# Performance work log

Measured on AMD Instinct MI355X. Metric: run time of the kernel, lower is better.

The kernel has to match this reference:

```python
import jax, jax.numpy as jnp
import numpy as np

LORA_ALPHA = 32.0
LORA_R = 16
SCALING = LORA_ALPHA / LORA_R


def setup_inputs() -> dict:
    key = jax.random.key(0)
    k1, k2, k3, k4, k5, k6 = jax.random.split(key, 6)
    B, S, D_IN, D_OUT = 4, 2048, 4096, 4096
    x = jax.random.normal(k1, (B, S, D_IN), dtype=jnp.float32)
    # int8 weight stored as int8 (spec uses int32 range [-127,127])
    qweight = jax.random.randint(k2, (D_OUT, D_IN), -127, 128, dtype=jnp.int32).astype(jnp.int8)
    # per-output-channel dequant scales (bf16 in torch; fp32 here for reference fidelity)
    scales = jax.random.uniform(k3, (D_OUT,), dtype=jnp.float32, minval=0.5, maxval=1.5) * 0.01
    bias = jax.random.normal(k4, (D_OUT,), dtype=jnp.float32) * 0.02
    # kaiming-uniform-like init for lora_A, zeros for lora_B would kill the LoRA
    # branch; use small random lora_B so the add path is exercised.
    bound = 1.0 / np.sqrt(D_IN)
    lora_A = jax.random.uniform(k5, (LORA_R, D_IN), dtype=jnp.float32, minval=-bound, maxval=bound)
    lora_B = jax.random.normal(k6, (D_OUT, LORA_R), dtype=jnp.float32) * 0.01
    return {"x": x, "qweight": qweight, "scales": scales, "bias": bias,
            "lora_A": lora_A, "lora_B": lora_B}


def reference(x, qweight, scales, bias, lora_A, lora_B):
    # W8A16 dequant: per-output-channel scale on int8 weight [out, in]
    w = qweight.astype(x.dtype) * scales[:, None]           # [out, in]
    base = jnp.einsum('bsi,oi->bso', x, w) + bias           # F.linear(x, W, b)
    # LoRA low-rank correction: (x @ A^T) @ B^T * scaling
    lora = jnp.einsum('bsr,or->bso', jnp.einsum('bsi,ri->bsr', x, lora_A), lora_B)
    return base + lora * SCALING
```

## Files before the change

kernel.cpp:

```cpp
#include <hip/hip_runtime.h>

#define LORA_RANK 16
#define SCALING 2.0f

using bf16x8 = __attribute__((ext_vector_type(8))) __bf16;
using bf16x4 = __attribute__((ext_vector_type(4))) __bf16;
using f32x4  = __attribute__((ext_vector_type(4))) float;
using i32x4  = __attribute__((ext_vector_type(4))) int;

#define GLB(p) ((const __attribute__((address_space(1))) void*)(p))
#define LDS(p) ((__attribute__((address_space(3))) void*)(p))

__global__ __launch_bounds__(256) void lora_mat_kernel(
    const float* __restrict__ lA, const float* __restrict__ lB,
    float* __restrict__ L, int N, int K)
{
    const int i0 = blockIdx.x * 256;
    const int o0 = blockIdx.y * 64;
    const int t  = threadIdx.x;

    __shared__ float As[LORA_RANK][256];
    __shared__ float Bs[64][LORA_RANK];

    #pragma unroll
    for (int j = 0; j < 16; ++j) {
        int idx = t + j * 256;
        int r = idx >> 8, c = idx & 255;
        As[r][c] = lA[(long)r * K + i0 + c];
    }
    #pragma unroll
    for (int j = 0; j < 4; ++j) {
        int idx = t + j * 256;
        int o = idx >> 4, r = idx & 15;
        Bs[o][r] = lB[(long)(o0 + o) * LORA_RANK + r] * SCALING;
    }
    __syncthreads();

    const int ol = t & 63;
    const int iq = t >> 6;
    const int o  = o0 + ol;

    float bb[LORA_RANK];
    #pragma unroll
    for (int r = 0; r < LORA_RANK; ++r) bb[r] = Bs[ol][r];

    float* lrow = L + (long)o * K + i0 + iq * 64;
    #pragma unroll
    for (int c = 0; c < 16; ++c) {
        const int ib = iq * 64 + c * 4;
        f32x4 v = {0.f, 0.f, 0.f, 0.f};
        #pragma unroll
        for (int r = 0; r < LORA_RANK; ++r) {
            v[0] += bb[r] * As[r][ib + 0];
            v[1] += bb[r] * As[r][ib + 1];
            v[2] += bb[r] * As[r][ib + 2];
            v[3] += bb[r] * As[r][ib + 3];
        }
        *(f32x4*)(lrow + c * 4) = v;
    }
}

__global__ __launch_bounds__(256) void quant_w_kernel(
    const int* __restrict__ q, const float* __restrict__ scales,
    const float* __restrict__ L, signed char* __restrict__ W8,
    float* __restrict__ sn, int K)
{
    const int o = blockIdx.x, t = threadIdx.x;
    __shared__ float buf[4096];
    __shared__ float red[256];

    const int4*  qr = (const int4*)(q + (long)o * K);
    const f32x4* Lr = (const f32x4*)(L + (long)o * K);
    const float  s  = scales[o];

    float mx = 0.f;
    #pragma unroll
    for (int j = 0; j < 4; ++j) {
        int c = t + j * 256;
        int4  qv = qr[c];
        f32x4 lv = Lr[c];
        f32x4 w;
        w[0] = (float)qv.x * s + lv[0];
        w[1] = (float)qv.y * s + lv[1];
        w[2] = (float)qv.z * s + lv[2];
        w[3] = (float)qv.w * s + lv[3];
        *(f32x4*)&buf[c * 4] = w;
        mx = fmaxf(mx, fmaxf(fmaxf(fabsf(w[0]), fabsf(w[1])),
                             fmaxf(fabsf(w[2]), fabsf(w[3]))));
    }
    red[t] = mx;
    __syncthreads();
    for (int s2 = 128; s2 > 0; s2 >>= 1) {
        if (t < s2) red[t] = fmaxf(red[t], red[t + s2]);
        __syncthreads();
    }
    const float gmax = fmaxf(red[0], 1e-30f);
    const float winv = 127.0f / gmax;

    int* wrow = (int*)(W8 + (long)o * K);
    #pragma unroll
    for (int j = 0; j < 4; ++j) {
        int c = t + j * 256;
        f32x4 w = *(const f32x4*)&buf[c * 4];
        int c0 = (int)rintf(fminf(fmaxf(w[0] * winv, -127.f), 127.f));
        int c1 = (int)rintf(fminf(fmaxf(w[1] * winv, -127.f), 127.f));
        int c2 = (int)rintf(fminf(fmaxf(w[2] * winv, -127.f), 127.f));
        int c3 = (int)rintf(fminf(fmaxf(w[3] * winv, -127.f), 127.f));
        wrow[c] = (c0 & 255) | ((c1 & 255) << 8) | ((c2 & 255) << 16) | (c3 << 24);
    }
    if (t == 0) sn[o] = gmax / 127.0f;
}

__global__ __launch_bounds__(256) void quant_x_kernel(
    const float* __restrict__ X, signed char* __restrict__ X8,
    float* __restrict__ sxm, int K)
{
    const int m = blockIdx.x, t = threadIdx.x;
    __shared__ float red[256];

    const f32x4* xr = (const f32x4*)(X + (long)m * K);
    f32x4 v[4];
    float mx = 0.f;
    #pragma unroll
    for (int j = 0; j < 4; ++j) {
        v[j] = xr[t + j * 256];
        mx = fmaxf(mx, fmaxf(fmaxf(fabsf(v[j][0]), fabsf(v[j][1])),
                             fmaxf(fabsf(v[j][2]), fabsf(v[j][3]))));
    }
    red[t] = mx;
    __syncthreads();
    for (int s2 = 128; s2 > 0; s2 >>= 1) {
        if (t < s2) red[t] = fmaxf(red[t], red[t + s2]);
        __syncthreads();
    }
    const float gmax = fmaxf(red[0], 1e-30f);
    const float xinv = 127.0f / gmax;

    int* xrow = (int*)(X8 + (long)m * K);
    #pragma unroll
    for (int j = 0; j < 4; ++j) {
        int c0 = (int)rintf(fminf(fmaxf(v[j][0] * xinv, -127.f), 127.f));
        int c1 = (int)rintf(fminf(fmaxf(v[j][1] * xinv, -127.f), 127.f));
        int c2 = (int)rintf(fminf(fmaxf(v[j][2] * xinv, -127.f), 127.f));
        int c3 = (int)rintf(fminf(fmaxf(v[j][3] * xinv, -127.f), 127.f));
        xrow[t + j * 256] = (c0 & 255) | ((c1 & 255) << 8) | ((c2 & 255) << 16) | (c3 << 24);
    }
    if (t == 0) sxm[m] = gmax / 127.0f;
}

#define VMW0  asm volatile("s_waitcnt vmcnt(0)" ::: "memory")
#define SB0   __builtin_amdgcn_sched_barrier(0)

#define RD4(base, off) (*(const i32x4*)((base) + (off)))

#define MFI(mi, nj, A, B) \
    acc[mi][nj] = __builtin_amdgcn_mfma_i32_16x16x64_i8(A, B, acc[mi][nj], 0, 0, 0)

#define STAGE_I8(dA, dB) do { \
    __builtin_amdgcn_global_load_lds(GLB(pB0), LDS((dB) + wb),        16, 0, 0); \
    __builtin_amdgcn_global_load_lds(GLB(pB1), LDS((dB) + wb + 8192), 16, 0, 0); \
    __builtin_amdgcn_global_load_lds(GLB(pA0), LDS((dA) + wb),        16, 0, 0); \
    __builtin_amdgcn_global_load_lds(GLB(pA1), LDS((dA) + wb + 8192), 16, 0, 0); } while (0)

#define ADVP8(a) do { pA0 += (a); pA1 += (a); pB0 += (a); pB1 += (a); } while (0)

#define TILE_I8(Ac, Bc, DOSTAGE) do { \
    const char* _ac = (Ac); const char* _bc = (Bc); \
    DOSTAGE; \
    i32x4 b0 = RD4(_bc, bRow +    0); \
    i32x4 b1 = RD4(_bc, bRow + 1024); \
    i32x4 b2 = RD4(_bc, bRow + 2048); \
    i32x4 b3 = RD4(_bc, bRow + 3072); \
    i32x4 a0 = RD4(_ac, aRow +    0); \
    i32x4 a1 = RD4(_ac, aRow + 1024); \
    i32x4 a2 = RD4(_ac, aRow + 2048); \
    i32x4 a3 = RD4(_ac, aRow + 3072); \
    i32x4 a4 = RD4(_ac, aRow + 4096); \
    i32x4 a5 = RD4(_ac, aRow + 5120); \
    i32x4 a6 = RD4(_ac, aRow + 6144); \
    i32x4 a7 = RD4(_ac, aRow + 7168); \
    __builtin_amdgcn_s_setprio(1); \
    MFI(0,0,a0,b0); MFI(1,0,a1,b0); MFI(2,0,a2,b0); MFI(3,0,a3,b0); \
    MFI(4,0,a4,b0); MFI(5,0,a5,b0); MFI(6,0,a6,b0); MFI(7,0,a7,b0); \
    MFI(0,1,a0,b1); MFI(1,1,a1,b1); MFI(2,1,a2,b1); MFI(3,1,a3,b1); \
    MFI(4,1,a4,b1); MFI(5,1,a5,b1); MFI(6,1,a6,b1); MFI(7,1,a7,b1); \
    MFI(0,2,a0,b2); MFI(1,2,a1,b2); MFI(2,2,a2,b2); MFI(3,2,a3,b2); \
    MFI(4,2,a4,b2); MFI(5,2,a5,b2); MFI(6,2,a6,b2); MFI(7,2,a7,b2); \
    MFI(0,3,a0,b3); MFI(1,3,a1,b3); MFI(2,3,a2,b3); MFI(3,3,a3,b3); \
    MFI(4,3,a4,b3); MFI(5,3,a5,b3); MFI(6,3,a6,b3); MFI(7,3,a7,b3); \
    __builtin_amdgcn_s_setprio(0); \
    VMW0; \
    __builtin_amdgcn_s_barrier(); \
    SB0; \
  } while (0)

__global__ __launch_bounds__(512, 2) void gemm_i8_kernel(
    const signed char* __restrict__ X8, const signed char* __restrict__ W8,
    const float* __restrict__ sxm, const float* __restrict__ sn,
    const float* __restrict__ bias, float* __restrict__ C,
    int M, int N, int K)
{
    __shared__ __align__(16) char smem[65536];

    const int t = threadIdx.x, wid = t >> 6, lane = t & 63;
    const int wr = wid >> 2, wc = wid & 3;
    const int l15 = lane & 15, lk = lane >> 4;

    const int nwg = gridDim.x;
    int bid = blockIdx.x;
    if ((nwg & 7) == 0) bid = (bid & 7) * (nwg >> 3) + (bid >> 3);
    const int ntn = N >> 8;
    const int m0 = (bid / ntn) << 8, n0 = (bid % ntn) << 8;

    const int sr = t >> 2, ch = t & 3;
    const signed char* pA0 = X8 + (long)(m0 +       sr) * K + ch * 16;
    const signed char* pA1 = X8 + (long)(m0 + 128 + sr) * K + ch * 16;
    const signed char* pB0 = W8 + (long)(n0 +       sr) * K + ch * 16;
    const signed char* pB1 = W8 + (long)(n0 + 128 + sr) * K + ch * 16;

    const int wb = wid * 1024;

    const int aRow = (wr * 128 + l15) * 64 + lk * 16;
    const int bRow = (wc * 64  + l15) * 64 + lk * 16;

    char* const bA0 = smem;
    char* const bB0 = smem + 16384;
    char* const bA1 = smem + 32768;
    char* const bB1 = smem + 49152;

    i32x4 acc[8][4] = {};

    const int nkt = K >> 6;

    STAGE_I8(bA0, bB0);
    ADVP8(nkt > 1 ? 64 : 0);
    VMW0;
    __builtin_amdgcn_s_barrier();
    SB0;

    for (int kt = 0; kt < nkt; kt += 2) {
        const long adv1 = (kt + 2 < nkt) ? 64 : 0;
        const long adv2 = (kt + 3 < nkt) ? 64 : 0;
        TILE_I8(bA0, bB0, { STAGE_I8(bA1, bB1); ADVP8(adv1); });
        TILE_I8(bA1, bB1, { STAGE_I8(bA0, bB0); ADVP8(adv2); });
    }

    #pragma unroll
    for (int nj = 0; nj < 4; ++nj) {
        const int col = n0 + wc * 64 + nj * 16 + l15;
        const float scol = sn[col];
        const float bv   = bias[col];
        #pragma unroll
        for (int mi = 0; mi < 8; ++mi) {
            const long rowb = (long)m0 + wr * 128 + mi * 16 + (lane >> 4) * 4;
            const f32x4 sx4 = *(const f32x4*)(sxm + rowb);
            float* Cp = C + rowb * N + col;
            Cp[0]       = (float)acc[mi][nj][0] * (sx4[0] * scol) + bv;
            Cp[(long)N] = (float)acc[mi][nj][1] * (sx4[1] * scol) + bv;
            Cp[2L * N]  = (float)acc[mi][nj][2] * (sx4[2] * scol) + bv;
            Cp[3L * N]  = (float)acc[mi][nj][3] * (sx4[3] * scol) + bv;
        }
    }
}

__global__ __launch_bounds__(256) void fold_weight_kernel(
    const int* __restrict__ q, const float* __restrict__ scales,
    const float* __restrict__ lA, const float* __restrict__ lB,
    __bf16* __restrict__ W, int N, int K)
{
    const int i0 = blockIdx.x * 256;
    const int o0 = blockIdx.y * 64;
    const int t  = threadIdx.x;

    __shared__ float As[LORA_RANK][256];
    __shared__ float Bs[64][LORA_RANK];

    #pragma unroll
    for (int j = 0; j < 16; ++j) {
        int idx = t + j * 256;
        As[idx >> 8][idx & 255] = lA[(long)(idx >> 8) * K + i0 + (idx & 255)];
    }
    #pragma unroll
    for (int j = 0; j < 4; ++j) {
        int idx = t + j * 256;
        Bs[idx >> 4][idx & 15] = lB[(long)(o0 + (idx >> 4)) * LORA_RANK + (idx & 15)] * SCALING;
    }
    __syncthreads();

    const int ol = t & 63, iq = t >> 6, o = o0 + ol;
    const float sc = scales[o];
    float bb[LORA_RANK];
    #pragma unroll
    for (int r = 0; r < LORA_RANK; ++r) bb[r] = Bs[ol][r];

    const int* qrow = q + (long)o * K + i0 + iq * 64;
    __bf16*    wrow = W + (long)o * K + i0 + iq * 64;
    #pragma unroll
    for (int c = 0; c < 16; ++c) {
        int4 q4 = *(const int4*)(qrow + c * 4);
        float v[4] = {(float)q4.x * sc, (float)q4.y * sc, (float)q4.z * sc, (float)q4.w * sc};
        const int ib = iq * 64 + c * 4;
        #pragma unroll
        for (int r = 0; r < LORA_RANK; ++r) {
            v[0] += bb[r] * As[r][ib + 0]; v[1] += bb[r] * As[r][ib + 1];
            v[2] += bb[r] * As[r][ib + 2]; v[3] += bb[r] * As[r][ib + 3];
        }
        bf16x4 wv; wv[0] = (__bf16)v[0]; wv[1] = (__bf16)v[1];
        wv[2] = (__bf16)v[2]; wv[3] = (__bf16)v[3];
        *(bf16x4*)(wrow + c * 4) = wv;
    }
}

__global__ __launch_bounds__(256) void cvt_x_kernel(
    const float* __restrict__ X, __bf16* __restrict__ Xb, long n)
{
    const long stride = (long)gridDim.x * 256 * 8;
    for (long i = ((long)blockIdx.x * 256 + threadIdx.x) * 8; i < n; i += stride) {
        f32x4 a = *(const f32x4*)(X + i);
        f32x4 b = *(const f32x4*)(X + i + 4);
        bf16x8 v;
        #pragma unroll
        for (int j = 0; j < 4; ++j) { v[j] = (__bf16)a[j]; v[j + 4] = (__bf16)b[j]; }
        *(bf16x8*)(Xb + i) = v;
    }
}

#define RD8(base, off) (*(const bf16x8*)((base) + (off)))
#define MF(mi, nj, A, B) \
    acc[mi][nj] = __builtin_amdgcn_mfma_f32_16x16x32_bf16(A, B, acc[mi][nj], 0, 0, 0)
#define SWEEP16(qb, A0, A1, A2, A3, B0, B1, B2, B3) \
    MF((qb)+0,0,A0,B0); MF((qb)+1,0,A1,B0); MF((qb)+2,0,A2,B0); MF((qb)+3,0,A3,B0); \
    MF((qb)+0,1,A0,B1); MF((qb)+1,1,A1,B1); MF((qb)+2,1,A2,B1); MF((qb)+3,1,A3,B1); \
    MF((qb)+0,2,A0,B2); MF((qb)+1,2,A1,B2); MF((qb)+2,2,A2,B2); MF((qb)+3,2,A3,B2); \
    MF((qb)+0,3,A0,B3); MF((qb)+1,3,A1,B3); MF((qb)+2,3,A2,B3); MF((qb)+3,3,A3,B3);
#define STAGE_ALL(dA, dB) do { \
    __builtin_amdgcn_global_load_lds(GLB(pB0),  LDS((dB) + wb),         16, 0, 0); \
    __builtin_amdgcn_global_load_lds(GLB(pB0b), LDS((dB) + wb +  8192), 16, 0, 0); \
    __builtin_amdgcn_global_load_lds(GLB(pB1),  LDS((dB) + wb + 16384), 16, 0, 0); \
    __builtin_amdgcn_global_load_lds(GLB(pB1b), LDS((dB) + wb + 24576), 16, 0, 0); \
    __builtin_amdgcn_global_load_lds(GLB(pA0),  LDS((dA) + wb),         16, 0, 0); \
    __builtin_amdgcn_global_load_lds(GLB(pA0b), LDS((dA) + wb +  8192), 16, 0, 0); \
    __builtin_amdgcn_global_load_lds(GLB(pA1),  LDS((dA) + wb + 16384), 16, 0, 0); \
    __builtin_amdgcn_global_load_lds(GLB(pA1b), LDS((dA) + wb + 24576), 16, 0, 0); } while (0)
#define ADVP(a) do { pA0 += (a); pA0b += (a); pA1 += (a); pA1b += (a); \
                     pB0 += (a); pB0b += (a); pB1 += (a); pB1b += (a); } while (0)
#define TILE3(Ac, Bc, DOSTAGE) do { \
    const char* _ac = (Ac); const char* _bc = (Bc); \
    DOSTAGE; \
    { bf16x8 b0 = RD8(_bc, bRow +    0 + kc0); bf16x8 b1 = RD8(_bc, bRow + 2048 + kc0); \
      bf16x8 b2 = RD8(_bc, bRow + 4096 + kc0); bf16x8 b3 = RD8(_bc, bRow + 6144 + kc0); \
      bf16x8 a0 = RD8(_ac, aRow +     0 + kc0); bf16x8 a1 = RD8(_ac, aRow +  2048 + kc0); \
      bf16x8 a2 = RD8(_ac, aRow +  4096 + kc0); bf16x8 a3 = RD8(_ac, aRow +  6144 + kc0); \
      bf16x8 a4 = RD8(_ac, aRow +  8192 + kc0); bf16x8 a5 = RD8(_ac, aRow + 10240 + kc0); \
      bf16x8 a6 = RD8(_ac, aRow + 12288 + kc0); bf16x8 a7 = RD8(_ac, aRow + 14336 + kc0); \
      __builtin_amdgcn_s_setprio(1); \
      SWEEP16(0, a0, a1, a2, a3, b0, b1, b2, b3); \
      SWEEP16(4, a4, a5, a6, a7, b0, b1, b2, b3); \
      __builtin_amdgcn_s_setprio(0); } \
    { bf16x8 b0 = RD8(_bc, bRow +    0 + kc1); bf16x8 b1 = RD8(_bc, bRow + 2048 + kc1); \
      bf16x8 b2 = RD8(_bc, bRow + 4096 + kc1); bf16x8 b3 = RD8(_bc, bRow + 6144 + kc1); \
      bf16x8 a0 = RD8(_ac, aRow +     0 + kc1); bf16x8 a1 = RD8(_ac, aRow +  2048 + kc1); \
      bf16x8 a2 = RD8(_ac, aRow +  4096 + kc1); bf16x8 a3 = RD8(_ac, aRow +  6144 + kc1); \
      bf16x8 a4 = RD8(_ac, aRow +  8192 + kc1); bf16x8 a5 = RD8(_ac, aRow + 10240 + kc1); \
      bf16x8 a6 = RD8(_ac, aRow + 12288 + kc1); bf16x8 a7 = RD8(_ac, aRow + 14336 + kc1); \
      __builtin_amdgcn_s_setprio(1); \
      SWEEP16(0, a0, a1, a2, a3, b0, b1, b2, b3); \
      SWEEP16(4, a4, a5, a6, a7, b0, b1, b2, b3); \
      __builtin_amdgcn_s_setprio(0); } \
    VMW0; \
    __builtin_amdgcn_s_barrier(); \
    SB0; \
  } while (0)

__global__ __launch_bounds__(512, 2) void gemm256_kernel(
    const __bf16* __restrict__ Xb, const __bf16* __restrict__ W,
    const float* __restrict__ bias, float* __restrict__ C,
    int M, int N, int K)
{
    __shared__ __align__(16) char smem[131072];

    const int t = threadIdx.x, wid = t >> 6, lane = t & 63;
    const int wr = wid >> 2, wc = wid & 3;
    const int l15 = lane & 15, l7 = lane & 7, lk = lane >> 4;

    const int nwg = gridDim.x;
    int bid = blockIdx.x;
    if ((nwg & 7) == 0) bid = (bid & 7) * (nwg >> 3) + (bid >> 3);
    const int ntn = N >> 8;
    const int m0 = (bid / ntn) << 8, n0 = (bid % ntn) << 8;

    const int sr = t >> 3;
    const int sc = (t & 7) ^ (sr & 7);
    const __bf16* pA0  = Xb + (long)(m0 +       sr) * K + sc * 8;
    const __bf16* pA0b = Xb + (long)(m0 +  64 + sr) * K + sc * 8;
    const __bf16* pA1  = Xb + (long)(m0 + 128 + sr) * K + sc * 8;
    const __bf16* pA1b = Xb + (long)(m0 + 192 + sr) * K + sc * 8;
    const __bf16* pB0  = W  + (long)(n0 +       sr) * K + sc * 8;
    const __bf16* pB0b = W  + (long)(n0 +  64 + sr) * K + sc * 8;
    const __bf16* pB1  = W  + (long)(n0 + 128 + sr) * K + sc * 8;
    const __bf16* pB1b = W  + (long)(n0 + 192 + sr) * K + sc * 8;

    const int wb = wid * 1024;
    const int aRow = (wr * 128 + l15) * 128;
    const int bRow = (wc * 64  + l15) * 128;
    const int kc0  = ((lk    ) ^ l7) << 4;
    const int kc1  = ((lk + 4) ^ l7) << 4;

    char* const bA0 = smem;
    char* const bB0 = smem + 32768;
    char* const bA1 = smem + 65536;
    char* const bB1 = smem + 98304;

    f32x4 acc[8][4] = {};
    const int nkt = K >> 6;

    STAGE_ALL(bA0, bB0);
    ADVP(nkt > 1 ? 64 : 0);
    VMW0;
    __builtin_amdgcn_s_barrier();
    SB0;

    for (int kt = 0; kt < nkt; kt += 2) {
        const long adv1 = (kt + 2 < nkt) ? 64 : 0;
        const long adv2 = (kt + 3 < nkt) ? 64 : 0;
        TILE3(bA0, bB0, { STAGE_ALL(bA1, bB1); ADVP(adv1); });
        TILE3(bA1, bB1, { STAGE_ALL(bA0, bB0); ADVP(adv2); });
    }

    #pragma unroll
    for (int nj = 0; nj < 4; ++nj) {
        const int col = n0 + wc * 64 + nj * 16 + l15;
        const float bv = bias[col];
        #pragma unroll
        for (int mi = 0; mi < 8; ++mi) {
            const long row = (long)m0 + wr * 128 + mi * 16 + (lane >> 4) * 4;
            float* Cp = C + row * N + col;
            Cp[0]       = acc[mi][nj][0] + bv;
            Cp[(long)N] = acc[mi][nj][1] + bv;
            Cp[2L * N]  = acc[mi][nj][2] + bv;
            Cp[3L * N]  = acc[mi][nj][3] + bv;
        }
    }
}

__global__ __launch_bounds__(256) void fallback_gemm(
    const float* __restrict__ X, const int* __restrict__ q,
    const float* __restrict__ scales, const float* __restrict__ bias,
    const float* __restrict__ lA, const float* __restrict__ lB,
    float* __restrict__ C, int M, int N, int K)
{
    __shared__ float Xs[64][17];
    __shared__ float Ws[64][17];
    __shared__ float At[LORA_RANK][16];
    __shared__ float Bt[64][LORA_RANK];

    const int ntn = N >> 6;
    const int m0 = (blockIdx.x / ntn) << 6, n0 = (blockIdx.x % ntn) << 6;
    const int t = threadIdx.x;

    for (int j = t; j < 64 * LORA_RANK; j += 256)
        Bt[j >> 4][j & 15] = lB[(long)(n0 + (j >> 4)) * LORA_RANK + (j & 15)] * SCALING;

    const int tr = (t & 15) * 4, tc = (t >> 4) * 4;
    float acc[4][4] = {};

    for (int k0 = 0; k0 < K; k0 += 16) {
        __syncthreads();
        for (int j = t; j < 1024; j += 256)
            Xs[j >> 4][j & 15] = X[(long)(m0 + (j >> 4)) * K + k0 + (j & 15)];
        At[t >> 4][t & 15] = lA[(long)(t >> 4) * K + k0 + (t & 15)];
        __syncthreads();
        for (int j = t; j < 1024; j += 256) {
            int o = j >> 4, kk = j & 15;
            float v = (float)q[(long)(n0 + o) * K + k0 + kk] * scales[n0 + o];
            #pragma unroll
            for (int r = 0; r < LORA_RANK; ++r) v += Bt[o][r] * At[r][kk];
            Ws[o][kk] = v;
        }
        __syncthreads();
        #pragma unroll 4
        for (int kk = 0; kk < 16; ++kk)
            #pragma unroll
            for (int i = 0; i < 4; ++i)
                #pragma unroll
                for (int j = 0; j < 4; ++j)
                    acc[i][j] += Xs[tr + i][kk] * Ws[tc + j][kk];
    }
    __syncthreads();
    #pragma unroll
    for (int i = 0; i < 4; ++i)
        #pragma unroll
        for (int j = 0; j < 4; ++j)
            C[(long)(m0 + tr + i) * N + n0 + tc + j] = acc[i][j] + bias[n0 + tc + j];
}

extern "C" void kernel_launch(void* const* d_in, const int* in_sizes, int n_in,
                              void* d_out, int out_size, void* d_ws, size_t ws_size,
                              hipStream_t stream)
{
    const float* x      = (const float*)d_in[0];
    const int*   qw     = (const int*)d_in[1];
    const float* scales = (const float*)d_in[2];
    const float* bias   = (const float*)d_in[3];
    const float* lA     = (const float*)d_in[4];
    const float* lB     = (const float*)d_in[5];
    float*       out    = (float*)d_out;

    const int K = in_sizes[4] / LORA_RANK;
    const int N = in_sizes[2];
    const int M = in_sizes[0] / K;

    const size_t i8need = (size_t)N * K + (size_t)M * K + (size_t)(M + N) * 4 + 256;
    const bool i8_ok = (K == 4096) && (M % 256) == 0 && (N % 256) == 0 &&
                       ((K >> 6) % 2) == 0 && (long)M * N >= (long)N * K &&
                       ws_size >= i8need;
    const size_t wbytes = (size_t)N * K * sizeof(__bf16);
    const size_t xbytes = (size_t)M * K * sizeof(__bf16);
    const bool big_ok = (M % 256) == 0 && (N % 256) == 0 && (K % 256) == 0 &&
                        ((K >> 6) % 2) == 0 && ws_size >= wbytes + xbytes;

    if (i8_ok) {
        signed char* W8  = (signed char*)d_ws;
        signed char* X8  = W8 + (size_t)N * K;
        float*       sxm = (float*)(X8 + (size_t)M * K);
        float*       sn  = sxm + M;
        float*       L   = out;

        dim3 g1(K / 256, N / 64);
        lora_mat_kernel<<<g1, 256, 0, stream>>>(lA, lB, L, N, K);
        quant_w_kernel<<<N, 256, 0, stream>>>(qw, scales, L, W8, sn, K);
        quant_x_kernel<<<M, 256, 0, stream>>>(x, X8, sxm, K);
        const int nwg = (M / 256) * (N / 256);
        gemm_i8_kernel<<<nwg, 512, 0, stream>>>(X8, W8, sxm, sn, bias, out, M, N, K);
    } else if (big_ok) {
        __bf16* W  = (__bf16*)d_ws;
        __bf16* Xb = (__bf16*)((char*)d_ws + wbytes);
        dim3 g1(K / 256, N / 64);
        fold_weight_kernel<<<g1, 256, 0, stream>>>(qw, scales, lA, lB, W, N, K);
        cvt_x_kernel<<<2048, 256, 0, stream>>>(x, Xb, (long)M * K);
        const int nwg = (M / 256) * (N / 256);
        gemm256_kernel<<<nwg, 512, 0, stream>>>(Xb, W, bias, out, M, N, K);
    } else {
        fallback_gemm<<<(M / 64) * (N / 64), 256, 0, stream>>>(
            x, qw, scales, bias, lA, lB, out, M, N, K);
    }
}
```

Measured before the change: 239.4 us.

## Deepen int8 GEMM K-tile to 128 with XOR-swizzled LDS, store LoRA delta as bf16

```diff
diff --git a/kernel.cpp b/kernel.cpp
--- a/kernel.cpp
+++ b/kernel.cpp
@@ -13,7 +13,7 @@
 
 __global__ __launch_bounds__(256) void lora_mat_kernel(
     const float* __restrict__ lA, const float* __restrict__ lB,
-    float* __restrict__ L, int N, int K)
+    __bf16* __restrict__ L, int N, int K)
 {
     const int i0 = blockIdx.x * 256;
     const int o0 = blockIdx.y * 64;
@@ -44,7 +44,7 @@
     #pragma unroll
     for (int r = 0; r < LORA_RANK; ++r) bb[r] = Bs[ol][r];
 
-    float* lrow = L + (long)o * K + i0 + iq * 64;
+    __bf16* lrow = L + (long)o * K + i0 + iq * 64;
     #pragma unroll
     for (int c = 0; c < 16; ++c) {
         const int ib = iq * 64 + c * 4;
@@ -56,34 +56,37 @@
             v[2] += bb[r] * As[r][ib + 2];
             v[3] += bb[r] * As[r][ib + 3];
         }
-        *(f32x4*)(lrow + c * 4) = v;
+        bf16x4 wv;
+        wv[0] = (__bf16)v[0]; wv[1] = (__bf16)v[1];
+        wv[2] = (__bf16)v[2]; wv[3] = (__bf16)v[3];
+        *(bf16x4*)(lrow + c * 4) = wv;
     }
 }
 
 __global__ __launch_bounds__(256) void quant_w_kernel(
     const int* __restrict__ q, const float* __restrict__ scales,
-    const float* __restrict__ L, signed char* __restrict__ W8,
+    const __bf16* __restrict__ L, signed char* __restrict__ W8,
     float* __restrict__ sn, int K)
 {
     const int o = blockIdx.x, t = threadIdx.x;
     __shared__ float buf[4096];
     __shared__ float red[256];
 
-    const int4*  qr = (const int4*)(q + (long)o * K);
-    const f32x4* Lr = (const f32x4*)(L + (long)o * K);
-    const float  s  = scales[o];
+    const int4*   qr = (const int4*)(q + (long)o * K);
+    const bf16x4* Lr = (const bf16x4*)(L + (long)o * K);
+    const float   s  = scales[o];
 
     float mx = 0.f;
     #pragma unroll
     for (int j = 0; j < 4; ++j) {
         int c = t + j * 256;
-        int4  qv = qr[c];
-        f32x4 lv = Lr[c];
+        int4   qv = qr[c];
+        bf16x4 lv = Lr[c];
         f32x4 w;
-        w[0] = (float)qv.x * s + lv[0];
-        w[1] = (float)qv.y * s + lv[1];
-        w[2] = (float)qv.z * s + lv[2];
-        w[3] = (float)qv.w * s + lv[3];
+        w[0] = (float)qv.x * s + (float)lv[0];
+        w[1] = (float)qv.y * s + (float)lv[1];
+        w[2] = (float)qv.z * s + (float)lv[2];
+        w[3] = (float)qv.w * s + (float)lv[3];
         *(f32x4*)&buf[c * 4] = w;
         mx = fmaxf(mx, fmaxf(fmaxf(fabsf(w[0]), fabsf(w[1])),
                              fmaxf(fabsf(w[2]), fabsf(w[3]))));
@@ -157,38 +160,68 @@
     acc[mi][nj] = __builtin_amdgcn_mfma_i32_16x16x64_i8(A, B, acc[mi][nj], 0, 0, 0)
 
 #define STAGE_I8(dA, dB) do { \
-    __builtin_amdgcn_global_load_lds(GLB(pB0), LDS((dB) + wb),        16, 0, 0); \
-    __builtin_amdgcn_global_load_lds(GLB(pB1), LDS((dB) + wb + 8192), 16, 0, 0); \
-    __builtin_amdgcn_global_load_lds(GLB(pA0), LDS((dA) + wb),        16, 0, 0); \
-    __builtin_amdgcn_global_load_lds(GLB(pA1), LDS((dA) + wb + 8192), 16, 0, 0); } while (0)
-
-#define ADVP8(a) do { pA0 += (a); pA1 += (a); pB0 += (a); pB1 += (a); } while (0)
+    __builtin_amdgcn_global_load_lds(GLB(pB),          LDS((dB) + wb),         16, 0, 0); \
+    __builtin_amdgcn_global_load_lds(GLB(pB + rk),     LDS((dB) + wb +  8192), 16, 0, 0); \
+    __builtin_amdgcn_global_load_lds(GLB(pB + 2 * rk), LDS((dB) + wb + 16384), 16, 0, 0); \
+    __builtin_amdgcn_global_load_lds(GLB(pB + 3 * rk), LDS((dB) + wb + 24576), 16, 0, 0); \
+    __builtin_amdgcn_global_load_lds(GLB(pA),          LDS((dA) + wb),         16, 0, 0); \
+    __builtin_amdgcn_global_load_lds(GLB(pA + rk),     LDS((dA) + wb +  8192), 16, 0, 0); \
+    __builtin_amdgcn_global_load_lds(GLB(pA + 2 * rk), LDS((dA) + wb + 16384), 16, 0, 0); \
+    __builtin_amdgcn_global_load_lds(GLB(pA + 3 * rk), LDS((dA) + wb + 24576), 16, 0, 0); } while (0)
+
+#define ADVP8(a) do { pA += (a); pB += (a); } while (0)
 
 #define TILE_I8(Ac, Bc, DOSTAGE) do { \
     const char* _ac = (Ac); const char* _bc = (Bc); \
     DOSTAGE; \
-    i32x4 b0 = RD4(_bc, bRow +    0); \
-    i32x4 b1 = RD4(_bc, bRow + 1024); \
-    i32x4 b2 = RD4(_bc, bRow + 2048); \
-    i32x4 b3 = RD4(_bc, bRow + 3072); \
-    i32x4 a0 = RD4(_ac, aRow +    0); \
-    i32x4 a1 = RD4(_ac, aRow + 1024); \
-    i32x4 a2 = RD4(_ac, aRow + 2048); \
-    i32x4 a3 = RD4(_ac, aRow + 3072); \
-    i32x4 a4 = RD4(_ac, aRow + 4096); \
-    i32x4 a5 = RD4(_ac, aRow + 5120); \
-    i32x4 a6 = RD4(_ac, aRow + 6144); \
-    i32x4 a7 = RD4(_ac, aRow + 7168); \
-    __builtin_amdgcn_s_setprio(1); \
-    MFI(0,0,a0,b0); MFI(1,0,a1,b0); MFI(2,0,a2,b0); MFI(3,0,a3,b0); \
-    MFI(4,0,a4,b0); MFI(5,0,a5,b0); MFI(6,0,a6,b0); MFI(7,0,a7,b0); \
-    MFI(0,1,a0,b1); MFI(1,1,a1,b1); MFI(2,1,a2,b1); MFI(3,1,a3,b1); \
-    MFI(4,1,a4,b1); MFI(5,1,a5,b1); MFI(6,1,a6,b1); MFI(7,1,a7,b1); \
-    MFI(0,2,a0,b2); MFI(1,2,a1,b2); MFI(2,2,a2,b2); MFI(3,2,a3,b2); \
-    MFI(4,2,a4,b2); MFI(5,2,a5,b2); MFI(6,2,a6,b2); MFI(7,2,a7,b2); \
-    MFI(0,3,a0,b3); MFI(1,3,a1,b3); MFI(2,3,a2,b3); MFI(3,3,a3,b3); \
-    MFI(4,3,a4,b3); MFI(5,3,a5,b3); MFI(6,3,a6,b3); MFI(7,3,a7,b3); \
-    __builtin_amdgcn_s_setprio(0); \
+    {  \
+      i32x4 b0 = RD4(_bc, bRow +    0 + kc0); \
+      i32x4 b1 = RD4(_bc, bRow + 2048 + kc0); \
+      i32x4 b2 = RD4(_bc, bRow + 4096 + kc0); \
+      i32x4 b3 = RD4(_bc, bRow + 6144 + kc0); \
+      i32x4 a0 = RD4(_ac, aRow +     0 + kc0); \
+      i32x4 a1 = RD4(_ac, aRow +  2048 + kc0); \
+      i32x4 a2 = RD4(_ac, aRow +  4096 + kc0); \
+      i32x4 a3 = RD4(_ac, aRow +  6144 + kc0); \
+      i32x4 a4 = RD4(_ac, aRow +  8192 + kc0); \
+      i32x4 a5 = RD4(_ac, aRow + 10240 + kc0); \
+      i32x4 a6 = RD4(_ac, aRow + 12288 + kc0); \
+      i32x4 a7 = RD4(_ac, aRow + 14336 + kc0); \
+      __builtin_amdgcn_s_setprio(1); \
+      MFI(0,0,a0,b0); MFI(1,0,a1,b0); MFI(2,0,a2,b0); MFI(3,0,a3,b0); \
+      MFI(4,0,a4,b0); MFI(5,0,a5,b0); MFI(6,0,a6,b0); MFI(7,0,a7,b0); \
+      MFI(0,1,a0,b1); MFI(1,1,a1,b1); MFI(2,1,a2,b1); MFI(3,1,a3,b1); \
+      MFI(4,1,a4,b1); MFI(5,1,a5,b1); MFI(6,1,a6,b1); MFI(7,1,a7,b1); \
+      MFI(0,2,a0,b2); MFI(1,2,a1,b2); MFI(2,2,a2,b2); MFI(3,2,a3,b2); \
+      MFI(4,2,a4,b2); MFI(5,2,a5,b2); MFI(6,2,a6,b2); MFI(7,2,a7,b2); \
+      MFI(0,3,a0,b3); MFI(1,3,a1,b3); MFI(2,3,a2,b3); MFI(3,3,a3,b3); \
+      MFI(4,3,a4,b3); MFI(5,3,a5,b3); MFI(6,3,a6,b3); MFI(7,3,a7,b3); \
+      __builtin_amdgcn_s_setprio(0); \
+    } \
+    {  \
+      i32x4 b0 = RD4(_bc, bRow +    0 + kc1); \
+      i32x4 b1 = RD4(_bc, bRow + 2048 + kc1); \
+      i32x4 b2 = RD4(_bc, bRow + 4096 + kc1); \
+      i32x4 b3 = RD4(_bc, bRow + 6144 + kc1); \
+      i32x4 a0 = RD4(_ac, aRow +     0 + kc1); \
+      i32x4 a1 = RD4(_ac, aRow +  2048 + kc1); \
+      i32x4 a2 = RD4(_ac, aRow +  4096 + kc1); \
+      i32x4 a3 = RD4(_ac, aRow +  6144 + kc1); \
+      i32x4 a4 = RD4(_ac, aRow +  8192 + kc1); \
+      i32x4 a5 = RD4(_ac, aRow + 10240 + kc1); \
+      i32x4 a6 = RD4(_ac, aRow + 12288 + kc1); \
+      i32x4 a7 = RD4(_ac, aRow + 14336 + kc1); \
+      __builtin_amdgcn_s_setprio(1); \
+      MFI(0,0,a0,b0); MFI(1,0,a1,b0); MFI(2,0,a2,b0); MFI(3,0,a3,b0); \
+      MFI(4,0,a4,b0); MFI(5,0,a5,b0); MFI(6,0,a6,b0); MFI(7,0,a7,b0); \
+      MFI(0,1,a0,b1); MFI(1,1,a1,b1); MFI(2,1,a2,b1); MFI(3,1,a3,b1); \
+      MFI(4,1,a4,b1); MFI(5,1,a5,b1); MFI(6,1,a6,b1); MFI(7,1,a7,b1); \
+      MFI(0,2,a0,b2); MFI(1,2,a1,b2); MFI(2,2,a2,b2); MFI(3,2,a3,b2); \
+      MFI(4,2,a4,b2); MFI(5,2,a5,b2); MFI(6,2,a6,b2); MFI(7,2,a7,b2); \
+      MFI(0,3,a0,b3); MFI(1,3,a1,b3); MFI(2,3,a2,b3); MFI(3,3,a3,b3); \
+      MFI(4,3,a4,b3); MFI(5,3,a5,b3); MFI(6,3,a6,b3); MFI(7,3,a7,b3); \
+      __builtin_amdgcn_s_setprio(0); \
+    } \
     VMW0; \
     __builtin_amdgcn_s_barrier(); \
     SB0; \
@@ -200,11 +233,11 @@
     const float* __restrict__ bias, float* __restrict__ C,
     int M, int N, int K)
 {
-    __shared__ __align__(16) char smem[65536];
+    __shared__ __align__(16) char smem[131072];
 
     const int t = threadIdx.x, wid = t >> 6, lane = t & 63;
     const int wr = wid >> 2, wc = wid & 3;
-    const int l15 = lane & 15, lk = lane >> 4;
+    const int l15 = lane & 15, l7 = lane & 7, lk = lane >> 4;
 
     const int nwg = gridDim.x;
     int bid = blockIdx.x;
@@ -212,35 +245,37 @@
     const int ntn = N >> 8;
     const int m0 = (bid / ntn) << 8, n0 = (bid % ntn) << 8;
 
-    const int sr = t >> 2, ch = t & 3;
-    const signed char* pA0 = X8 + (long)(m0 +       sr) * K + ch * 16;
-    const signed char* pA1 = X8 + (long)(m0 + 128 + sr) * K + ch * 16;
-    const signed char* pB0 = W8 + (long)(n0 +       sr) * K + ch * 16;
-    const signed char* pB1 = W8 + (long)(n0 + 128 + sr) * K + ch * 16;
+    const int sr = t >> 3;
+    const int ch = (t & 7) ^ (sr & 7);
+    const long rk = 64L * K;
+    const signed char* pA = X8 + (long)(m0 + sr) * K + ch * 16;
+    const signed char* pB = W8 + (long)(n0 + sr) * K + ch * 16;
 
     const int wb = wid * 1024;
 
-    const int aRow = (wr * 128 + l15) * 64 + lk * 16;
-    const int bRow = (wc * 64  + l15) * 64 + lk * 16;
+    const int aRow = (wr * 128 + l15) * 128;
+    const int bRow = (wc * 64  + l15) * 128;
+    const int kc0  = ((lk    ) ^ l7) << 4;
+    const int kc1  = ((lk + 4) ^ l7) << 4;
 
     char* const bA0 = smem;
-    char* const bB0 = smem + 16384;
-    char* const bA1 = smem + 32768;
-    char* const bB1 = smem + 49152;
+    char* const bB0 = smem + 32768;
+    char* const bA1 = smem + 65536;
+    char* const bB1 = smem + 98304;
 
     i32x4 acc[8][4] = {};
 
-    const int nkt = K >> 6;
+    const int nkt = K >> 7;
 
     STAGE_I8(bA0, bB0);
-    ADVP8(nkt > 1 ? 64 : 0);
+    ADVP8(nkt > 1 ? 128 : 0);
     VMW0;
     __builtin_amdgcn_s_barrier();
     SB0;
 
     for (int kt = 0; kt < nkt; kt += 2) {
-        const long adv1 = (kt + 2 < nkt) ? 64 : 0;
-        const long adv2 = (kt + 3 < nkt) ? 64 : 0;
+        const long adv1 = (kt + 2 < nkt) ? 128 : 0;
+        const long adv2 = (kt + 3 < nkt) ? 128 : 0;
         TILE_I8(bA0, bB0, { STAGE_I8(bA1, bB1); ADVP8(adv1); });
         TILE_I8(bA1, bB1, { STAGE_I8(bA0, bB0); ADVP8(adv2); });
     }
@@ -510,9 +545,9 @@
     const int N = in_sizes[2];
     const int M = in_sizes[0] / K;
 
-    const size_t i8need = (size_t)N * K + (size_t)M * K + (size_t)(M + N) * 4 + 256;
+    const size_t i8need = (size_t)N * K + (size_t)M * K + (size_t)(M + N) * 4
+                        + (size_t)N * K * 2 + 256;
     const bool i8_ok = (K == 4096) && (M % 256) == 0 && (N % 256) == 0 &&
-                       ((K >> 6) % 2) == 0 && (long)M * N >= (long)N * K &&
                        ws_size >= i8need;
     const size_t wbytes = (size_t)N * K * sizeof(__bf16);
     const size_t xbytes = (size_t)M * K * sizeof(__bf16);
@@ -524,7 +559,7 @@
         signed char* X8  = W8 + (size_t)N * K;
         float*       sxm = (float*)(X8 + (size_t)M * K);
         float*       sn  = sxm + M;
-        float*       L   = out;
+        __bf16*      L   = (__bf16*)(sn + N);
 
         dim3 g1(K / 256, N / 64);
         lora_mat_kernel<<<g1, 256, 0, stream>>>(lA, lB, L, N, K);
```

Result: faster. 220.0 us (-8.1%).
